# Kernel tuning notes

Hardware: AMD Instinct MI355X
Metric: run time of the kernel (lower is better)

## Reference

```python
import jax, jax.numpy as jnp
import numpy as np

N = 2048       # nodes (also onehot length)
E = 32768      # edges (avg degree 16)
C_IN = 128
C_OUT = 128
OH_CH = 8
BN_EPS = 1e-5


def _conv1d(x, w):
    # x: [N, Cin, L], w: [Cout, Cin, 3], padding 1 (SAME)
    return jax.lax.conv_general_dilated(
        x, w, window_strides=(1,), padding=[(1, 1)],
        dimension_numbers=('NCH', 'OIH', 'NCH'))


def setup_inputs() -> dict:
    key = jax.random.key(0)
    ks = jax.random.split(key, 16)
    x = jax.random.normal(ks[0], (N, C_IN), dtype=jnp.float32)
    onehot = jax.random.uniform(ks[1], (N, N), dtype=jnp.float32)
    adj = jax.random.randint(ks[2], (2, E), 0, N)

    def lin(k, fan_in, shape):
        return jax.random.normal(k, shape, dtype=jnp.float32) / np.sqrt(fan_in)

    # first_linear: (C_IN + OH_CH) -> C_OUT  (stored as [in, out])
    W1 = lin(ks[3], C_IN + OH_CH, (C_IN + OH_CH, C_OUT))
    b1 = jnp.zeros((C_OUT,), jnp.float32)
    # mlp: BatchNorm1d(C_OUT) -> ReLU -> Linear(C_OUT, C_OUT)
    gamma = jnp.ones((C_OUT,), jnp.float32)
    beta = jnp.zeros((C_OUT,), jnp.float32)
    W2 = lin(ks[4], C_OUT, (C_OUT, C_OUT))
    b2 = jnp.zeros((C_OUT,), jnp.float32)
    # onehot_pipe: Conv1d(1,8,3) -> ReLU -> Conv1d(8,16,3) -> ReLU -> avgpool -> Linear(16, OH_CH)
    cw1 = lin(ks[5], 1 * 3, (8, 1, 3)); cb1 = jnp.zeros((8,), jnp.float32)
    cw2 = lin(ks[6], 8 * 3, (16, 8, 3)); cb2 = jnp.zeros((16,), jnp.float32)
    Wr = lin(ks[7], 16, (16, OH_CH)); br = jnp.zeros((OH_CH,), jnp.float32)

    return {"x": x, "onehot": onehot, "adj": adj, "n_nodes": N,
            "W1": W1, "b1": b1, "gamma": gamma, "beta": beta,
            "W2": W2, "b2": b2, "cw1": cw1, "cb1": cb1,
            "cw2": cw2, "cb2": cb2, "Wr": Wr, "br": br}


def reference(x, onehot, adj, n_nodes, W1, b1, gamma, beta, W2, b2,
              cw1, cb1, cw2, cb2, Wr, br):
    send, recv = adj[0], adj[1]
    # propagate: gather at senders, scatter-add at receivers
    agg_x = jax.ops.segment_sum(x[send], recv, num_segments=n_nodes)          # [N, C_IN]
    agg_oh = jax.ops.segment_sum(onehot[send], recv, num_segments=n_nodes)    # [N, N]
    new_oh = onehot + agg_oh                                                  # update()

    # onehot_pipe on sorted onehot rows
    s = jnp.sort(new_oh, axis=-1)[:, None, :]                                 # [N, 1, L]
    h = jax.nn.relu(_conv1d(s, cw1) + cb1[None, :, None])                     # [N, 8, L]
    h = jax.nn.relu(_conv1d(h, cw2) + cb2[None, :, None])                     # [N, 16, L]
    h = h.mean(axis=-1)                                                       # AdaptiveAvgPool1d(1)+Flatten
    readout = h @ Wr + br                                                     # [N, OH_CH]

    x2 = jnp.concatenate([agg_x, readout], axis=1)                            # hstack
    x2 = x2 @ W1 + b1                                                         # first_linear
    # BatchNorm1d in training mode (batch stats, biased variance)
    mu = x2.mean(axis=0)
    var = x2.var(axis=0)
    x2 = (x2 - mu) * jax.lax.rsqrt(var + BN_EPS) * gamma + beta
    x2 = jax.nn.relu(x2)
    x2 = x2 @ W2 + b2
    return (x2, new_oh)
```

## Files before the change

kernel.cpp:

```cpp
#include <hip/hip_runtime.h>
#include <hip/hip_bf16.h>
#include <math.h>

#define NN   2048
#define LROW 2048
#define DEGCAP 128

typedef __attribute__((ext_vector_type(8))) short short8;
typedef __attribute__((ext_vector_type(4))) float f32x4;

__device__ __forceinline__ unsigned short bf16b(float x) {
    __hip_bfloat16 h = __float2bfloat16(x);
    return *reinterpret_cast<unsigned short*>(&h);
}


__global__ void fill2_k(const int* __restrict__ send, const int* __restrict__ recv,
                        int* __restrict__ cnt, int* __restrict__ elist2, int E) {
    int i = blockIdx.x * blockDim.x + threadIdx.x;
    if (i >= E) return;
    int r = recv[i];
    int slot = atomicAdd(&cnt[r], 1);
    if (slot < DEGCAP) elist2[r * DEGCAP + slot] = send[i];
}


__global__ __launch_bounds__(256) void oh2bf_k(const float* __restrict__ oh,
                                               unsigned short* __restrict__ ohbf) {
    int base = blockIdx.x * 2048 + threadIdx.x * 8;
    float4 f0 = *(const float4*)(oh + base);
    float4 f1 = *(const float4*)(oh + base + 4);
    union { short8 s8; unsigned short us[8]; } pk;
    pk.us[0] = bf16b(f0.x); pk.us[1] = bf16b(f0.y);
    pk.us[2] = bf16b(f0.z); pk.us[3] = bf16b(f0.w);
    pk.us[4] = bf16b(f1.x); pk.us[5] = bf16b(f1.y);
    pk.us[6] = bf16b(f1.z); pk.us[7] = bf16b(f1.w);
    *(short8*)(ohbf + base) = pk.s8;
}


__device__ __forceinline__ void ce(float& a, float& b, bool up) {
    float lo = fminf(a, b), hi = fmaxf(a, b);
    a = up ? lo : hi;
    b = up ? hi : lo;
}

__device__ __forceinline__ void merge8(float v[8], bool up) {
    ce(v[0], v[4], up); ce(v[1], v[5], up); ce(v[2], v[6], up); ce(v[3], v[7], up);
    ce(v[0], v[2], up); ce(v[1], v[3], up); ce(v[4], v[6], up); ce(v[5], v[7], up);
    ce(v[0], v[1], up); ce(v[2], v[3], up); ce(v[4], v[5], up); ce(v[6], v[7], up);
}

__device__ __forceinline__ short8 conv1pack(float xm, float x0v, float xp,
        const float* __restrict__ cw1, const float* __restrict__ cb1) {
    union { short8 s8; unsigned short us[8]; } pk;
#pragma unroll
    for (int c = 0; c < 8; ++c) {
        float w = cb1[c] + cw1[c * 3] * xm + cw1[c * 3 + 1] * x0v + cw1[c * 3 + 2] * xp;
        pk.us[c] = bf16b(w > 0.f ? w : 0.f);
    }
    return pk.s8;
}


template<int BF>
__global__ __launch_bounds__(256, 6) void fused_k(
        const float* __restrict__ oh, const unsigned short* __restrict__ ohbf,
        const float* __restrict__ x,
        const int* __restrict__ elist2, const int* __restrict__ cnt,
        float* __restrict__ newoh, float* __restrict__ t,
        const float* __restrict__ cw1, const float* __restrict__ cb1,
        const float* __restrict__ cw2, const float* __restrict__ cb2,
        const float* __restrict__ Wr,  const float* __restrict__ br,
        const float* __restrict__ W1,  const float* __restrict__ b1) {
    __shared__ __align__(16) char smem[1028 * 16];
    float* sf = (float*)smem;
    unsigned short* h1t = (unsigned short*)smem;
    __shared__ unsigned short a_lds[16 * 32];
    __shared__ float red[4][16];
    __shared__ float u[136];
    __shared__ float lpart[128];

    const int r = blockIdx.x, tid = threadIdx.x;
    const int lane = tid & 63, wv = tid >> 6;
    const int col = tid * 8;

    for (int i = tid; i < 512; i += 256) {
        int c2 = i >> 5, k = i & 31, d = k >> 3, c1 = k & 7;
        float w = (d < 3) ? cw2[(c2 * 8 + c1) * 3 + d] : 0.f;
        a_lds[i] = bf16b(w);
    }

    float v[8];
    {
        float4 b0 = *(const float4*)(oh + (size_t)r * LROW + col);
        float4 b1v = *(const float4*)(oh + (size_t)r * LROW + col + 4);
        v[0] = b0.x;  v[1] = b0.y;  v[2] = b0.z;  v[3] = b0.w;
        v[4] = b1v.x; v[5] = b1v.y; v[6] = b1v.z; v[7] = b1v.w;
    }
    float myagg = 0.f;
    const int deg = min(cnt[r], DEGCAP);
    const int* my = elist2 + r * DEGCAP;
    int e = 0;
    if (BF) {
        for (; e + 2 <= deg; e += 2) {
            int se0 = my[e], se1 = my[e + 1];
            uint4 ua = *(const uint4*)((const unsigned*)(ohbf + (size_t)se0 * LROW) + tid * 4);
            uint4 ub = *(const uint4*)((const unsigned*)(ohbf + (size_t)se1 * LROW) + tid * 4);
            float xa = 0.f, xb = 0.f;
            if (tid < 128) { xa = x[(size_t)se0 * 128 + tid]; xb = x[(size_t)se1 * 128 + tid]; }
            v[0] += __uint_as_float(ua.x << 16); v[1] += __uint_as_float(ua.x & 0xffff0000u);
            v[2] += __uint_as_float(ua.y << 16); v[3] += __uint_as_float(ua.y & 0xffff0000u);
            v[4] += __uint_as_float(ua.z << 16); v[5] += __uint_as_float(ua.z & 0xffff0000u);
            v[6] += __uint_as_float(ua.w << 16); v[7] += __uint_as_float(ua.w & 0xffff0000u);
            v[0] += __uint_as_float(ub.x << 16); v[1] += __uint_as_float(ub.x & 0xffff0000u);
            v[2] += __uint_as_float(ub.y << 16); v[3] += __uint_as_float(ub.y & 0xffff0000u);
            v[4] += __uint_as_float(ub.z << 16); v[5] += __uint_as_float(ub.z & 0xffff0000u);
            v[6] += __uint_as_float(ub.w << 16); v[7] += __uint_as_float(ub.w & 0xffff0000u);
            myagg += xa; myagg += xb;
        }
        for (; e < deg; ++e) {
            int se = my[e];
            uint4 ua = *(const uint4*)((const unsigned*)(ohbf + (size_t)se * LROW) + tid * 4);
            if (tid < 128) myagg += x[(size_t)se * 128 + tid];
            v[0] += __uint_as_float(ua.x << 16); v[1] += __uint_as_float(ua.x & 0xffff0000u);
            v[2] += __uint_as_float(ua.y << 16); v[3] += __uint_as_float(ua.y & 0xffff0000u);
            v[4] += __uint_as_float(ua.z << 16); v[5] += __uint_as_float(ua.z & 0xffff0000u);
            v[6] += __uint_as_float(ua.w << 16); v[7] += __uint_as_float(ua.w & 0xffff0000u);
        }
    } else {
        for (; e + 2 <= deg; e += 2) {
            int se0 = my[e], se1 = my[e + 1];
            float4 c0 = *(const float4*)(oh + (size_t)se0 * LROW + col);
            float4 c1 = *(const float4*)(oh + (size_t)se0 * LROW + col + 4);
            float4 d0 = *(const float4*)(oh + (size_t)se1 * LROW + col);
            float4 d1 = *(const float4*)(oh + (size_t)se1 * LROW + col + 4);
            float xa = 0.f, xb = 0.f;
            if (tid < 128) { xa = x[(size_t)se0 * 128 + tid]; xb = x[(size_t)se1 * 128 + tid]; }
            v[0] += c0.x; v[1] += c0.y; v[2] += c0.z; v[3] += c0.w;
            v[4] += c1.x; v[5] += c1.y; v[6] += c1.z; v[7] += c1.w;
            v[0] += d0.x; v[1] += d0.y; v[2] += d0.z; v[3] += d0.w;
            v[4] += d1.x; v[5] += d1.y; v[6] += d1.z; v[7] += d1.w;
            myagg += xa; myagg += xb;
        }
        for (; e < deg; ++e) {
            int se = my[e];
            float4 c0 = *(const float4*)(oh + (size_t)se * LROW + col);
            float4 c1 = *(const float4*)(oh + (size_t)se * LROW + col + 4);
            if (tid < 128) myagg += x[(size_t)se * 128 + tid];
            v[0] += c0.x; v[1] += c0.y; v[2] += c0.z; v[3] += c0.w;
            v[4] += c1.x; v[5] += c1.y; v[6] += c1.z; v[7] += c1.w;
        }
    }
    *(float4*)(newoh + (size_t)r * LROW + col)     = make_float4(v[0], v[1], v[2], v[3]);
    *(float4*)(newoh + (size_t)r * LROW + col + 4) = make_float4(v[4], v[5], v[6], v[7]);

    ce(v[0], v[1], true);  ce(v[2], v[3], false); ce(v[4], v[5], true);  ce(v[6], v[7], false);
    ce(v[0], v[2], true);  ce(v[1], v[3], true);  ce(v[4], v[6], false); ce(v[5], v[7], false);
    ce(v[0], v[1], true);  ce(v[2], v[3], true);  ce(v[4], v[5], false); ce(v[6], v[7], false);
    merge8(v, (tid & 1) == 0);

#pragma unroll
    for (int lk = 4; lk <= 11; ++lk) {
        const int k = 1 << lk;
        const bool up = ((tid & (k >> 3)) == 0);
#pragma unroll
        for (int lj = lk - 1; lj >= 3; --lj) {
            const int j = 1 << lj;
            const int D = j >> 3;
            const bool keepmin = (((tid & D) == 0) == up);
            if (D <= 32) {
#pragma unroll
                for (int q = 0; q < 8; ++q) {
                    float rr = __shfl_xor(v[q], D, 64);
                    float mn = fminf(v[q], rr), mx = fmaxf(v[q], rr);
                    v[q] = keepmin ? mn : mx;
                }
            } else {
                __syncthreads();
                *(float4*)&sf[col]     = make_float4(v[0], v[1], v[2], v[3]);
                *(float4*)&sf[col + 4] = make_float4(v[4], v[5], v[6], v[7]);
                __syncthreads();
                const int pc = (tid ^ D) * 8;
                float4 A = *(const float4*)&sf[pc];
                float4 B = *(const float4*)&sf[pc + 4];
                float rr[8] = {A.x, A.y, A.z, A.w, B.x, B.y, B.z, B.w};
#pragma unroll
                for (int q = 0; q < 8; ++q) {
                    float mn = fminf(v[q], rr[q]), mx = fmaxf(v[q], rr[q]);
                    v[q] = keepmin ? mn : mx;
                }
            }
        }
        merge8(v, up);
    }

    __syncthreads();
    *(float4*)&sf[col]     = make_float4(v[0], v[1], v[2], v[3]);
    *(float4*)&sf[col + 4] = make_float4(v[4], v[5], v[6], v[7]);
    __syncthreads();
    float lf1 = (tid == 0)   ? 0.f : sf[col - 1];
    float rt1 = (tid == 255) ? 0.f : sf[col + 8];

    short8 afrag = *(const short8*)&a_lds[(lane & 15) * 32 + (lane >> 4) * 8];
    const int mb = (lane >> 4) * 4;
    const float bs0 = cb2[mb], bs1 = cb2[mb + 1], bs2 = cb2[mb + 2], bs3 = cb2[mb + 3];
    float s0 = 0.f, s1 = 0.f, s2 = 0.f, s3 = 0.f;
    f32x4 zero = {0.f, 0.f, 0.f, 0.f};

#pragma unroll 1
    for (int half = 0; half < 2; ++half) {
        __syncthreads();
        if ((tid >> 7) == half) {
            const int lt = tid & 127;
#pragma unroll
            for (int p = 0; p < 8; ++p) {
                float xm  = (p == 0) ? lf1 : v[p - 1];
                float x0v = v[p];
                float xp  = (p == 7) ? rt1 : v[p + 1];
                int uu = lt * 8 + p + 1;
                int us = uu ^ ((uu >> 3) & 7);
                *(short8*)&h1t[us * 8] = conv1pack(xm, x0v, xp, cw1, cb1);
            }
        }
        if (half == 0) {
            if (tid == 128)
                *(short8*)&h1t[1025 * 8] = conv1pack(lf1, v[0], v[1], cw1, cb1);
            if (tid == 0) {
                short8 z = {0, 0, 0, 0, 0, 0, 0, 0};
                *(short8*)&h1t[0] = z;
            }
            if (tid == 1) {
                short8 z = {0, 0, 0, 0, 0, 0, 0, 0};
                *(short8*)&h1t[1026 * 8] = z;
                *(short8*)&h1t[1027 * 8] = z;
            }
        } else {
            if (tid == 127)
                *(short8*)&h1t[0] = conv1pack(v[6], v[7], rt1, cw1, cb1);
            if (tid == 0) {
                short8 z = {0, 0, 0, 0, 0, 0, 0, 0};
                *(short8*)&h1t[1025 * 8] = z;
            }
        }
        __syncthreads();

#pragma unroll 4
        for (int i = 0; i < 16; ++i) {
            int lp = (wv * 16 + i) * 16 + (lane & 15);
            int uu = lp + (lane >> 4);
            int us = uu ^ ((uu >> 3) & 7);
            short8 bfrag = *(const short8*)&h1t[us * 8];
            f32x4 d = __builtin_amdgcn_mfma_f32_16x16x32_bf16(afrag, bfrag, zero, 0, 0, 0);
            s0 += fmaxf(d[0] + bs0, 0.f);
            s1 += fmaxf(d[1] + bs1, 0.f);
            s2 += fmaxf(d[2] + bs2, 0.f);
            s3 += fmaxf(d[3] + bs3, 0.f);
        }
    }

#pragma unroll
    for (int off = 1; off < 16; off <<= 1) {
        s0 += __shfl_xor(s0, off);
        s1 += __shfl_xor(s1, off);
        s2 += __shfl_xor(s2, off);
        s3 += __shfl_xor(s3, off);
    }
    if ((lane & 15) == 0) {
        red[wv][mb + 0] = s0; red[wv][mb + 1] = s1;
        red[wv][mb + 2] = s2; red[wv][mb + 3] = s3;
    }
    if (tid < 128) u[tid] = myagg;
    __syncthreads();

    if (tid < 8) {
        float acc = br[tid];
#pragma unroll
        for (int c = 0; c < 16; ++c) {
            float tot = red[0][c] + red[1][c] + red[2][c] + red[3][c];
            acc += (tot * (1.0f / (float)LROW)) * Wr[c * 8 + tid];
        }
        u[128 + tid] = acc;
    }
    __syncthreads();

    {
        const int jc = tid & 127, hf = tid >> 7;
        float acc = (hf == 0) ? b1[jc] : 0.f;
        const int c0 = hf * 68;
#pragma unroll 4
        for (int c = 0; c < 68; ++c) acc += u[c0 + c] * W1[(size_t)(c0 + c) * 128 + jc];
        if (hf) lpart[jc] = acc;
        __syncthreads();
        if (!hf) t[(size_t)r * 128 + jc] = acc + lpart[jc];
    }
}


__global__ __launch_bounds__(256) void bnpart_k(const float* __restrict__ t,
                                                float* __restrict__ part) {
    const int b = blockIdx.x, tid = threadIdx.x;
    const int col = tid & 127, h = tid >> 7;
    float sm = 0.f, sq = 0.f;
    for (int i = 0; i < 32; ++i) {
        int row = b * 64 + h * 32 + i;
        float v = t[(size_t)row * 128 + col];
        sm += v; sq += v * v;
    }
    __shared__ float ps[2][128], pq[2][128];
    ps[h][col] = sm; pq[h][col] = sq;
    __syncthreads();
    if (h == 0) {
        part[(size_t)b * 256 + col]       = sm + ps[1][col];
        part[(size_t)b * 256 + 128 + col] = sq + pq[1][col];
    }
}

__global__ void bnfin_k(const float* __restrict__ part,
                        const float* __restrict__ gamma, const float* __restrict__ beta,
                        float* __restrict__ bnst) {
    int j = threadIdx.x;
    float sm = 0.f, sq = 0.f;
    for (int b = 0; b < 32; ++b) {
        sm += part[(size_t)b * 256 + j];
        sq += part[(size_t)b * 256 + 128 + j];
    }
    float mu  = sm / (float)NN;
    float var = sq / (float)NN - mu * mu;
    float sc  = rsqrtf(var + 1e-5f) * gamma[j];
    bnst[j] = sc;
    bnst[128 + j] = beta[j] - mu * sc;
}


__global__ __launch_bounds__(256) void out_k(
        float* __restrict__ t, const float* __restrict__ bnst,
        const float* __restrict__ W2, const float* __restrict__ b2) {
    __shared__ float u[16][128];
    const int r0 = blockIdx.x * 16, tid = threadIdx.x;
#pragma unroll
    for (int m = 0; m < 8; ++m) {
        int idx = tid + 256 * m;
        int rr = idx >> 7, c = idx & 127;
        float v = t[(size_t)(r0 + rr) * 128 + c];
        v = v * bnst[c] + bnst[128 + c];
        u[rr][c] = v > 0.f ? v : 0.f;
    }
    __syncthreads();
    const int j = tid & 127, g = tid >> 7;
    float acc[8];
    float bb = b2[j];
#pragma unroll
    for (int rr = 0; rr < 8; ++rr) acc[rr] = bb;
    for (int c = 0; c < 128; ++c) {
        float w = W2[(size_t)c * 128 + j];
#pragma unroll
        for (int rr = 0; rr < 8; ++rr) acc[rr] += u[g * 8 + rr][c] * w;
    }
#pragma unroll
    for (int rr = 0; rr < 8; ++rr)
        t[(size_t)(r0 + g * 8 + rr) * 128 + j] = acc[rr];
}


extern "C" void kernel_launch(void* const* d_in, const int* in_sizes, int n_in,
                              void* d_out, int out_size, void* d_ws, size_t ws_size,
                              hipStream_t stream) {
    const float* x      = (const float*)d_in[0];
    const float* onehot = (const float*)d_in[1];
    const int*   adj    = (const int*)d_in[2];
    const float* W1     = (const float*)d_in[4];
    const float* b1     = (const float*)d_in[5];
    const float* gamma  = (const float*)d_in[6];
    const float* beta   = (const float*)d_in[7];
    const float* W2     = (const float*)d_in[8];
    const float* b2     = (const float*)d_in[9];
    const float* cw1    = (const float*)d_in[10];
    const float* cb1    = (const float*)d_in[11];
    const float* cw2    = (const float*)d_in[12];
    const float* cb2    = (const float*)d_in[13];
    const float* Wr     = (const float*)d_in[14];
    const float* br     = (const float*)d_in[15];

    const int E = in_sizes[2] / 2;
    const int* send = adj;
    const int* recv = adj + E;

    int*   cnt    = (int*)d_ws;
    int*   elist2 = cnt + 2048;
    float* bnst   = (float*)(elist2 + NN * DEGCAP);
    float* part   = bnst + 256;
    unsigned short* ohbf = (unsigned short*)(part + 32 * 256);
    size_t need = (size_t)((char*)(ohbf + (size_t)NN * LROW) - (char*)d_ws);
    const bool bf_path = (ws_size >= need);

    float* out_x2 = (float*)d_out;
    float* out_oh = out_x2 + (size_t)NN * 128;

    hipMemsetAsync(cnt, 0, 2048 * sizeof(int), stream);

    fill2_k<<<(E + 255) / 256, 256, 0, stream>>>(send, recv, cnt, elist2, E);
    if (bf_path) {
        oh2bf_k<<<NN, 256, 0, stream>>>(onehot, ohbf);
        fused_k<1><<<NN, 256, 0, stream>>>(onehot, ohbf, x, elist2, cnt,
                                           out_oh, out_x2,
                                           cw1, cb1, cw2, cb2, Wr, br, W1, b1);
    } else {
        fused_k<0><<<NN, 256, 0, stream>>>(onehot, ohbf, x, elist2, cnt,
                                           out_oh, out_x2,
                                           cw1, cb1, cw2, cb2, Wr, br, W1, b1);
    }
    bnpart_k<<<32, 256, 0, stream>>>(out_x2, part);
    bnfin_k<<<1, 128, 0, stream>>>(part, gamma, beta, bnst);
    out_k<<<NN / 16, 256, 0, stream>>>(out_x2, bnst, W2, b2);
}
```

Before: 95.50 us.

## Pack bitonic sort into fp16 pairs, merge prep kernels, fold BN finalize into output

The bitonic sort of each onehot row now runs on packed fp16 pairs using v_pk_min/max. This halves the shuffle and compare count, and the LDS exchange becomes one uint4 per thread. The bf16 conversion and edge-list build are merged into a single prep kernel, and the BN finalize kernel is folded into out_k, with each block recomputing the stats. The gather loop is unrolled to 4 edges. The fp16 sort lowers the precision of the sorted values feeding the conv and may exceed tolerance, and the recomputed BN stats add redundant work per block.

```diff
diff --git a/kernel.cpp b/kernel.cpp
--- a/kernel.cpp
+++ b/kernel.cpp
@@ -8,12 +8,57 @@
 
 typedef __attribute__((ext_vector_type(8))) short short8;
 typedef __attribute__((ext_vector_type(4))) float f32x4;
+typedef unsigned int u32;
 
 __device__ __forceinline__ unsigned short bf16b(float x) {
     __hip_bfloat16 h = __float2bfloat16(x);
     return *reinterpret_cast<unsigned short*>(&h);
 }
 
+
+__device__ __forceinline__ u32 pkmin(u32 a, u32 b) {
+    u32 d; asm("v_pk_min_f16 %0, %1, %2" : "=v"(d) : "v"(a), "v"(b)); return d;
+}
+__device__ __forceinline__ u32 pkmax(u32 a, u32 b) {
+    u32 d; asm("v_pk_max_f16 %0, %1, %2" : "=v"(d) : "v"(a), "v"(b)); return d;
+}
+__device__ __forceinline__ u32 packf2(float lo, float hi) {
+    union { _Float16 h[2]; u32 u; } c;
+    c.h[0] = (_Float16)lo; c.h[1] = (_Float16)hi;
+    return c.u;
+}
+__device__ __forceinline__ float unpk_lo(u32 v) {
+    union { u32 u; _Float16 h[2]; } c; c.u = v; return (float)c.h[0];
+}
+__device__ __forceinline__ float unpk_hi(u32 v) {
+    union { u32 u; _Float16 h[2]; } c; c.u = v; return (float)c.h[1];
+}
+
+
+__global__ __launch_bounds__(256) void prep_k(
+        const float* __restrict__ oh, unsigned short* __restrict__ ohbf,
+        const int* __restrict__ send, const int* __restrict__ recv,
+        int* __restrict__ cnt, int* __restrict__ elist2, int E) {
+    const int bid = blockIdx.x;
+    if (bid < NN) {
+        int base = bid * 2048 + threadIdx.x * 8;
+        float4 f0 = *(const float4*)(oh + base);
+        float4 f1 = *(const float4*)(oh + base + 4);
+        union { short8 s8; unsigned short us[8]; } pk;
+        pk.us[0] = bf16b(f0.x); pk.us[1] = bf16b(f0.y);
+        pk.us[2] = bf16b(f0.z); pk.us[3] = bf16b(f0.w);
+        pk.us[4] = bf16b(f1.x); pk.us[5] = bf16b(f1.y);
+        pk.us[6] = bf16b(f1.z); pk.us[7] = bf16b(f1.w);
+        *(short8*)(ohbf + base) = pk.s8;
+    } else {
+        int i = (bid - NN) * 256 + threadIdx.x;
+        if (i < E) {
+            int r = recv[i];
+            int slot = atomicAdd(&cnt[r], 1);
+            if (slot < DEGCAP) elist2[r * DEGCAP + slot] = send[i];
+        }
+    }
+}
 
 __global__ void fill2_k(const int* __restrict__ send, const int* __restrict__ recv,
                         int* __restrict__ cnt, int* __restrict__ elist2, int E) {
@@ -25,30 +70,30 @@
 }
 
 
-__global__ __launch_bounds__(256) void oh2bf_k(const float* __restrict__ oh,
-                                               unsigned short* __restrict__ ohbf) {
-    int base = blockIdx.x * 2048 + threadIdx.x * 8;
-    float4 f0 = *(const float4*)(oh + base);
-    float4 f1 = *(const float4*)(oh + base + 4);
-    union { short8 s8; unsigned short us[8]; } pk;
-    pk.us[0] = bf16b(f0.x); pk.us[1] = bf16b(f0.y);
-    pk.us[2] = bf16b(f0.z); pk.us[3] = bf16b(f0.w);
-    pk.us[4] = bf16b(f1.x); pk.us[5] = bf16b(f1.y);
-    pk.us[6] = bf16b(f1.z); pk.us[7] = bf16b(f1.w);
-    *(short8*)(ohbf + base) = pk.s8;
-}
-
-
 __device__ __forceinline__ void ce(float& a, float& b, bool up) {
     float lo = fminf(a, b), hi = fmaxf(a, b);
     a = up ? lo : hi;
     b = up ? hi : lo;
 }
 
-__device__ __forceinline__ void merge8(float v[8], bool up) {
-    ce(v[0], v[4], up); ce(v[1], v[5], up); ce(v[2], v[6], up); ce(v[3], v[7], up);
-    ce(v[0], v[2], up); ce(v[1], v[3], up); ce(v[4], v[6], up); ce(v[5], v[7], up);
-    ce(v[0], v[1], up); ce(v[2], v[3], up); ce(v[4], v[5], up); ce(v[6], v[7], up);
+__device__ __forceinline__ void ce_pk(u32& a, u32& b, bool up) {
+    u32 mn = pkmin(a, b), mx = pkmax(a, b);
+    a = up ? mn : mx;
+    b = up ? mx : mn;
+}
+
+__device__ __forceinline__ void merge8_pk(u32 h[4], bool up) {
+    ce_pk(h[0], h[2], up); ce_pk(h[1], h[3], up);
+    ce_pk(h[0], h[1], up); ce_pk(h[2], h[3], up);
+#pragma unroll
+    for (int m = 0; m < 4; ++m) {
+        u32 hs = (h[m] >> 16) | (h[m] << 16);
+        u32 mn = pkmin(h[m], hs);
+        u32 mx = pkmax(h[m], hs);
+        u32 ru = __builtin_amdgcn_perm(mx, mn, 0x07060100u);
+        u32 rd = __builtin_amdgcn_perm(mn, mx, 0x07060100u);
+        h[m] = up ? ru : rd;
+    }
 }
 
 __device__ __forceinline__ short8 conv1pack(float xm, float x0v, float xp,
@@ -75,6 +120,7 @@
         const float* __restrict__ W1,  const float* __restrict__ b1) {
     __shared__ __align__(16) char smem[1028 * 16];
     float* sf = (float*)smem;
+    u32* sfu = (u32*)smem;
     unsigned short* h1t = (unsigned short*)smem;
     __shared__ unsigned short a_lds[16 * 32];
     __shared__ float red[4][16];
@@ -103,12 +149,17 @@
     const int* my = elist2 + r * DEGCAP;
     int e = 0;
     if (BF) {
-        for (; e + 2 <= deg; e += 2) {
-            int se0 = my[e], se1 = my[e + 1];
-            uint4 ua = *(const uint4*)((const unsigned*)(ohbf + (size_t)se0 * LROW) + tid * 4);
-            uint4 ub = *(const uint4*)((const unsigned*)(ohbf + (size_t)se1 * LROW) + tid * 4);
-            float xa = 0.f, xb = 0.f;
-            if (tid < 128) { xa = x[(size_t)se0 * 128 + tid]; xb = x[(size_t)se1 * 128 + tid]; }
+        for (; e + 4 <= deg; e += 4) {
+            int se0 = my[e], se1 = my[e + 1], se2 = my[e + 2], se3 = my[e + 3];
+            uint4 ua = *((const uint4*)(ohbf + (size_t)se0 * LROW) + tid);
+            uint4 ub = *((const uint4*)(ohbf + (size_t)se1 * LROW) + tid);
+            uint4 uc = *((const uint4*)(ohbf + (size_t)se2 * LROW) + tid);
+            uint4 ud = *((const uint4*)(ohbf + (size_t)se3 * LROW) + tid);
+            float xa = 0.f, xb = 0.f, xc = 0.f, xd = 0.f;
+            if (tid < 128) {
+                xa = x[(size_t)se0 * 128 + tid]; xb = x[(size_t)se1 * 128 + tid];
+                xc = x[(size_t)se2 * 128 + tid]; xd = x[(size_t)se3 * 128 + tid];
+            }
             v[0] += __uint_as_float(ua.x << 16); v[1] += __uint_as_float(ua.x & 0xffff0000u);
             v[2] += __uint_as_float(ua.y << 16); v[3] += __uint_as_float(ua.y & 0xffff0000u);
             v[4] += __uint_as_float(ua.z << 16); v[5] += __uint_as_float(ua.z & 0xffff0000u);
@@ -117,11 +168,19 @@
             v[2] += __uint_as_float(ub.y << 16); v[3] += __uint_as_float(ub.y & 0xffff0000u);
             v[4] += __uint_as_float(ub.z << 16); v[5] += __uint_as_float(ub.z & 0xffff0000u);
             v[6] += __uint_as_float(ub.w << 16); v[7] += __uint_as_float(ub.w & 0xffff0000u);
-            myagg += xa; myagg += xb;
+            v[0] += __uint_as_float(uc.x << 16); v[1] += __uint_as_float(uc.x & 0xffff0000u);
+            v[2] += __uint_as_float(uc.y << 16); v[3] += __uint_as_float(uc.y & 0xffff0000u);
+            v[4] += __uint_as_float(uc.z << 16); v[5] += __uint_as_float(uc.z & 0xffff0000u);
+            v[6] += __uint_as_float(uc.w << 16); v[7] += __uint_as_float(uc.w & 0xffff0000u);
+            v[0] += __uint_as_float(ud.x << 16); v[1] += __uint_as_float(ud.x & 0xffff0000u);
+            v[2] += __uint_as_float(ud.y << 16); v[3] += __uint_as_float(ud.y & 0xffff0000u);
+            v[4] += __uint_as_float(ud.z << 16); v[5] += __uint_as_float(ud.z & 0xffff0000u);
+            v[6] += __uint_as_float(ud.w << 16); v[7] += __uint_as_float(ud.w & 0xffff0000u);
+            myagg += xa; myagg += xb; myagg += xc; myagg += xd;
         }
         for (; e < deg; ++e) {
             int se = my[e];
-            uint4 ua = *(const uint4*)((const unsigned*)(ohbf + (size_t)se * LROW) + tid * 4);
+            uint4 ua = *((const uint4*)(ohbf + (size_t)se * LROW) + tid);
             if (tid < 128) myagg += x[(size_t)se * 128 + tid];
             v[0] += __uint_as_float(ua.x << 16); v[1] += __uint_as_float(ua.x & 0xffff0000u);
             v[2] += __uint_as_float(ua.y << 16); v[3] += __uint_as_float(ua.y & 0xffff0000u);
@@ -158,7 +217,18 @@
     ce(v[0], v[1], true);  ce(v[2], v[3], false); ce(v[4], v[5], true);  ce(v[6], v[7], false);
     ce(v[0], v[2], true);  ce(v[1], v[3], true);  ce(v[4], v[6], false); ce(v[5], v[7], false);
     ce(v[0], v[1], true);  ce(v[2], v[3], true);  ce(v[4], v[5], false); ce(v[6], v[7], false);
-    merge8(v, (tid & 1) == 0);
+    {
+        bool up8 = (tid & 1) == 0;
+        ce(v[0], v[4], up8); ce(v[1], v[5], up8); ce(v[2], v[6], up8); ce(v[3], v[7], up8);
+        ce(v[0], v[2], up8); ce(v[1], v[3], up8); ce(v[4], v[6], up8); ce(v[5], v[7], up8);
+        ce(v[0], v[1], up8); ce(v[2], v[3], up8); ce(v[4], v[5], up8); ce(v[6], v[7], up8);
+    }
+
+    u32 h[4];
+    h[0] = packf2(v[0], v[1]);
+    h[1] = packf2(v[2], v[3]);
+    h[2] = packf2(v[4], v[5]);
+    h[3] = packf2(v[6], v[7]);
 
 #pragma unroll
     for (int lk = 4; lk <= 11; ++lk) {
@@ -166,34 +236,33 @@
         const bool up = ((tid & (k >> 3)) == 0);
 #pragma unroll
         for (int lj = lk - 1; lj >= 3; --lj) {
-            const int j = 1 << lj;
-            const int D = j >> 3;
+            const int D = 1 << (lj - 3);
             const bool keepmin = (((tid & D) == 0) == up);
             if (D <= 32) {
 #pragma unroll
-                for (int q = 0; q < 8; ++q) {
-                    float rr = __shfl_xor(v[q], D, 64);
-                    float mn = fminf(v[q], rr), mx = fmaxf(v[q], rr);
-                    v[q] = keepmin ? mn : mx;
+                for (int m = 0; m < 4; ++m) {
+                    u32 hs = (u32)__shfl_xor((int)h[m], D, 64);
+                    u32 mn = pkmin(h[m], hs), mx = pkmax(h[m], hs);
+                    h[m] = keepmin ? mn : mx;
                 }
             } else {
                 __syncthreads();
-                *(float4*)&sf[col]     = make_float4(v[0], v[1], v[2], v[3]);
-                *(float4*)&sf[col + 4] = make_float4(v[4], v[5], v[6], v[7]);
+                *(uint4*)&sfu[tid * 4] = make_uint4(h[0], h[1], h[2], h[3]);
                 __syncthreads();
-                const int pc = (tid ^ D) * 8;
-                float4 A = *(const float4*)&sf[pc];
-                float4 B = *(const float4*)&sf[pc + 4];
-                float rr[8] = {A.x, A.y, A.z, A.w, B.x, B.y, B.z, B.w};
-#pragma unroll
-                for (int q = 0; q < 8; ++q) {
-                    float mn = fminf(v[q], rr[q]), mx = fmaxf(v[q], rr[q]);
-                    v[q] = keepmin ? mn : mx;
-                }
-            }
-        }
-        merge8(v, up);
-    }
+                uint4 P = *(const uint4*)&sfu[(tid ^ D) * 4];
+                h[0] = keepmin ? pkmin(h[0], P.x) : pkmax(h[0], P.x);
+                h[1] = keepmin ? pkmin(h[1], P.y) : pkmax(h[1], P.y);
+                h[2] = keepmin ? pkmin(h[2], P.z) : pkmax(h[2], P.z);
+                h[3] = keepmin ? pkmin(h[3], P.w) : pkmax(h[3], P.w);
+            }
+        }
+        merge8_pk(h, up);
+    }
+
+    v[0] = unpk_lo(h[0]); v[1] = unpk_hi(h[0]);
+    v[2] = unpk_lo(h[1]); v[3] = unpk_hi(h[1]);
+    v[4] = unpk_lo(h[2]); v[5] = unpk_hi(h[2]);
+    v[6] = unpk_lo(h[3]); v[7] = unpk_hi(h[3]);
 
     __syncthreads();
     *(float4*)&sf[col]     = make_float4(v[0], v[1], v[2], v[3]);
@@ -316,34 +385,33 @@
     }
 }
 
-__global__ void bnfin_k(const float* __restrict__ part,
-                        const float* __restrict__ gamma, const float* __restrict__ beta,
-                        float* __restrict__ bnst) {
-    int j = threadIdx.x;
-    float sm = 0.f, sq = 0.f;
-    for (int b = 0; b < 32; ++b) {
-        sm += part[(size_t)b * 256 + j];
-        sq += part[(size_t)b * 256 + 128 + j];
-    }
-    float mu  = sm / (float)NN;
-    float var = sq / (float)NN - mu * mu;
-    float sc  = rsqrtf(var + 1e-5f) * gamma[j];
-    bnst[j] = sc;
-    bnst[128 + j] = beta[j] - mu * sc;
-}
-
 
 __global__ __launch_bounds__(256) void out_k(
-        float* __restrict__ t, const float* __restrict__ bnst,
+        float* __restrict__ t, const float* __restrict__ part,
+        const float* __restrict__ gamma, const float* __restrict__ beta,
         const float* __restrict__ W2, const float* __restrict__ b2) {
     __shared__ float u[16][128];
+    __shared__ float sc_s[128], sh_s[128];
     const int r0 = blockIdx.x * 16, tid = threadIdx.x;
+    if (tid < 128) {
+        float sm = 0.f, sq = 0.f;
+        for (int b = 0; b < 32; ++b) {
+            sm += part[(size_t)b * 256 + tid];
+            sq += part[(size_t)b * 256 + 128 + tid];
+        }
+        float mu  = sm / (float)NN;
+        float var = sq / (float)NN - mu * mu;
+        float sc  = rsqrtf(var + 1e-5f) * gamma[tid];
+        sc_s[tid] = sc;
+        sh_s[tid] = beta[tid] - mu * sc;
+    }
+    __syncthreads();
 #pragma unroll
     for (int m = 0; m < 8; ++m) {
         int idx = tid + 256 * m;
         int rr = idx >> 7, c = idx & 127;
         float v = t[(size_t)(r0 + rr) * 128 + c];
-        v = v * bnst[c] + bnst[128 + c];
+        v = v * sc_s[c] + sh_s[c];
         u[rr][c] = v > 0.f ? v : 0.f;
     }
     __syncthreads();
@@ -388,8 +456,7 @@
 
     int*   cnt    = (int*)d_ws;
     int*   elist2 = cnt + 2048;
-    float* bnst   = (float*)(elist2 + NN * DEGCAP);
-    float* part   = bnst + 256;
+    float* part   = (float*)(elist2 + NN * DEGCAP);
     unsigned short* ohbf = (unsigned short*)(part + 32 * 256);
     size_t need = (size_t)((char*)(ohbf + (size_t)NN * LROW) - (char*)d_ws);
     const bool bf_path = (ws_size >= need);
@@ -399,18 +466,18 @@
 
     hipMemsetAsync(cnt, 0, 2048 * sizeof(int), stream);
 
-    fill2_k<<<(E + 255) / 256, 256, 0, stream>>>(send, recv, cnt, elist2, E);
     if (bf_path) {
-        oh2bf_k<<<NN, 256, 0, stream>>>(onehot, ohbf);
+        prep_k<<<NN + (E + 255) / 256, 256, 0, stream>>>(onehot, ohbf, send, recv,
+                                                         cnt, elist2, E);
         fused_k<1><<<NN, 256, 0, stream>>>(onehot, ohbf, x, elist2, cnt,
                                            out_oh, out_x2,
                                            cw1, cb1, cw2, cb2, Wr, br, W1, b1);
     } else {
+        fill2_k<<<(E + 255) / 256, 256, 0, stream>>>(send, recv, cnt, elist2, E);
         fused_k<0><<<NN, 256, 0, stream>>>(onehot, ohbf, x, elist2, cnt,
                                            out_oh, out_x2,
                                            cw1, cb1, cw2, cb2, Wr, br, W1, b1);
     }
     bnpart_k<<<32, 256, 0, stream>>>(out_x2, part);
-    bnfin_k<<<1, 128, 0, stream>>>(part, gamma, beta, bnst);
-    out_k<<<NN / 16, 256, 0, stream>>>(out_x2, bnst, W2, b2);
-}
+    out_k<<<NN / 16, 256, 0, stream>>>(out_x2, part, gamma, beta, W2, b2);
+}
```

Result: faster. 81.10 us (-15.1%).
